# Kernel optimization log

Measured on AMD Instinct MI355X. Metric: run time of the kernel, lower is better.

The kernel has to match this reference:

```python
import jax, jax.numpy as jnp
import numpy as np

DIM = 512
N_HEADS = 8
HEAD_DIM = DIM // N_HEADS
BN_EPS = 1e-5


def setup_inputs() -> dict:
    key = jax.random.key(0)
    ks = jax.random.split(key, 8)
    B, C, H, W = 16, DIM, 32, 32
    x = jax.random.normal(ks[0], (B, C, H, W), dtype=jnp.float32)
    # 1x1 convs == channel matmuls: stacked q/k/v weights [3, out, in], proj [out, in]
    w_qkv = jax.random.normal(ks[1], (3, DIM, DIM), dtype=jnp.float32) * (DIM ** -0.5)
    w_proj = jax.random.normal(ks[2], (DIM, DIM), dtype=jnp.float32) * (DIM ** -0.5)
    # BatchNorm (inference form) params for q/k/v branches, stacked [3, C]
    bn_gamma = jax.random.uniform(ks[3], (3, DIM), minval=0.5, maxval=1.5)
    bn_beta = jax.random.normal(ks[4], (3, DIM)) * 0.1
    bn_mean = jax.random.normal(ks[5], (3, DIM)) * 0.1
    bn_var = jax.random.uniform(ks[6], (3, DIM), minval=0.5, maxval=1.5)
    return {"x": x, "w_qkv": w_qkv, "w_proj": w_proj, "bn_gamma": bn_gamma,
            "bn_beta": bn_beta, "bn_mean": bn_mean, "bn_var": bn_var}


def _ternary_ste(t):
    # forward: sign(t) in {-1,0,1}; backward: identity (straight-through)
    return t + jax.lax.stop_gradient(jnp.sign(t) - t)


def reference(x, w_qkv, w_proj, bn_gamma, bn_beta, bn_mean, bn_var):
    B, C, H, W = x.shape
    N = H * W
    xf = x.reshape(B, C, N)
    # fused 1x1 conv for q,k,v: [3,B,C,N]
    qkv = jnp.einsum('koc,bcn->kbon', w_qkv, xf)
    # BatchNorm (inference): y = (x - mean)/sqrt(var+eps)*gamma + beta
    s = bn_gamma / jnp.sqrt(bn_var + BN_EPS)          # [3,C]
    b = bn_beta - bn_mean * s                          # [3,C]
    qkv = qkv * s[:, None, :, None] + b[:, None, :, None]
    q = _ternary_ste(qkv[0]).reshape(B, N_HEADS, HEAD_DIM, N)
    k = _ternary_ste(qkv[1]).reshape(B, N_HEADS, HEAD_DIM, N)
    v = qkv[2].reshape(B, N_HEADS, HEAD_DIM, N)
    scale = HEAD_DIM ** -0.5
    attn = jnp.einsum('bhdn,bhen->bhde', q, k) * scale  # [B,h,d,d] channel-wise attn
    attn = jax.nn.softmax(attn, axis=-1)
    out = jnp.einsum('bhde,bhen->bhdn', attn, v).reshape(B, C, N)
    out = jnp.einsum('oc,bcn->bon', w_proj, out) + xf   # proj + residual
    return out.reshape(B, C, H, W)
```

## Files before the change

### kernel.cpp

```cpp
#include <hip/hip_runtime.h>
#include <math.h>

#define BN_EPS 1e-5f
#define FIXC 1.0e-4f

typedef _Float16 f16;
typedef _Float16 f16x4 __attribute__((ext_vector_type(4)));
typedef _Float16 f16x8 __attribute__((ext_vector_type(8)));
typedef float f32x4 __attribute__((ext_vector_type(4)));
typedef int i32x4 __attribute__((ext_vector_type(4)));

static constexpr int BB = 16;
static constexpr int C  = 512;
static constexpr int NP = 1024;
static constexpr int NH = 8;
static constexpr int HD = 64;
static constexpr int M3 = 1536;


static constexpr size_t OFF_WHI  = 0;
static constexpr size_t OFF_WLO  = 1572864;
static constexpr size_t OFF_WPH  = 3145728;
static constexpr size_t OFF_SB   = 3670016;
static constexpr size_t OFF_WN   = 3682304;
static constexpr size_t OFF_XN   = 3686400;
static constexpr size_t OFF_FLAG = 3751936;
static constexpr size_t OFF_XTH  = 5849088;
static constexpr size_t OFF_XTL  = 22626304;
static constexpr size_t OFF_AOT  = OFF_XTH;
static constexpr size_t OFF_Q    = 39403520;
static constexpr size_t OFF_K    = 47792128;
static constexpr size_t OFF_VT   = 56180736;

__device__ __forceinline__ void gld16(const void* g, void* l) {
  __builtin_amdgcn_global_load_lds(
      (const __attribute__((address_space(1))) void*)g,
      (__attribute__((address_space(3))) void*)l, 16, 0, 0);
}

__device__ __forceinline__ size_t frag_off(int tile, int kt, int row7, int k5) {
  return (((size_t)tile * 16 + kt) * 8 + (row7 >> 4)) * 512
       + (size_t)((row7 & 15) | ((k5 >> 3) << 4)) * 8;
}

__global__ __launch_bounds__(256) void k_convW(
    const float* __restrict__ wqkv, const float* __restrict__ wproj,
    const float* __restrict__ g, const float* __restrict__ be,
    const float* __restrict__ mu, const float* __restrict__ va,
    f16* __restrict__ Whi, f16* __restrict__ Wlo, f16* __restrict__ Wph,
    float* __restrict__ sA, float* __restrict__ bA)
{
  const int i = blockIdx.x * 256 + threadIdx.x;
  {
    const int m = i >> 6, l = i & 63;
    const float4 v0 = *(const float4*)&wqkv[(size_t)m * C + l * 8];
    const float4 v1 = *(const float4*)&wqkv[(size_t)m * C + l * 8 + 4];
    const float vv[8] = {v0.x, v0.y, v0.z, v0.w, v1.x, v1.y, v1.z, v1.w};
    f16x8 hv, lv;
#pragma unroll
    for (int q = 0; q < 8; ++q) {
      const f16 h = (f16)vv[q];
      hv[q] = h; lv[q] = (f16)(vv[q] - (float)h);
    }
    *(f16x8*)&Whi[frag_off(m >> 7, l >> 2, m & 127, (l & 3) * 8)] = hv;
    *(f16x8*)&Wlo[(size_t)m * C + l * 8] = lv;
  }
  if (i < 32768) {
    const int m = i >> 6, l = i & 63;
    const float4 v0 = *(const float4*)&wproj[(size_t)m * C + l * 8];
    const float4 v1 = *(const float4*)&wproj[(size_t)m * C + l * 8 + 4];
    const float vv[8] = {v0.x, v0.y, v0.z, v0.w, v1.x, v1.y, v1.z, v1.w};
    f16x8 hv;
#pragma unroll
    for (int q = 0; q < 8; ++q) hv[q] = (f16)vv[q];
    *(f16x8*)&Wph[frag_off(m >> 7, l >> 2, m & 127, (l & 3) * 8)] = hv;
  }
  if (i < M3) {
    const float s = g[i] / sqrtf(va[i] + BN_EPS);
    sA[i] = s;
    bA[i] = be[i] - mu[i] * s;
  }
}

__global__ __launch_bounds__(256) void k_wnorm(
    const float* __restrict__ wqkv, float* __restrict__ wnorm)
{
  const int row = blockIdx.x * 4 + (threadIdx.x >> 6);
  const int lane = threadIdx.x & 63;
  const float4 v0 = *(const float4*)&wqkv[(size_t)row * C + lane * 8];
  const float4 v1 = *(const float4*)&wqkv[(size_t)row * C + lane * 8 + 4];
  float s = v0.x * v0.x + v0.y * v0.y + v0.z * v0.z + v0.w * v0.w
          + v1.x * v1.x + v1.y * v1.y + v1.z * v1.z + v1.w * v1.w;
  s += __shfl_xor(s, 1);  s += __shfl_xor(s, 2);  s += __shfl_xor(s, 4);
  s += __shfl_xor(s, 8);  s += __shfl_xor(s, 16); s += __shfl_xor(s, 32);
  if (lane == 0) wnorm[row] = sqrtf(s);
}

__global__ __launch_bounds__(256) void k_convX(
    const float* __restrict__ x, f16* __restrict__ XtH, f16* __restrict__ XtL,
    float* __restrict__ xnorm2)
{
  const int k0 = blockIdx.x * 64, n0 = blockIdx.y * 64, b = blockIdx.z;
  __shared__ float ls[64][65];
  const int t = threadIdx.x;
  const float* xp = x + ((size_t)b * C + k0) * NP + n0;
  const int c4 = (t & 15) * 4, r0 = t >> 4;
#pragma unroll
  for (int q = 0; q < 4; ++q) {
    const float4 v = *(const float4*)(xp + (size_t)(r0 + q * 16) * NP + c4);
    ls[r0 + q * 16][c4 + 0] = v.x; ls[r0 + q * 16][c4 + 1] = v.y;
    ls[r0 + q * 16][c4 + 2] = v.z; ls[r0 + q * 16][c4 + 3] = v.w;
  }
  __syncthreads();
  if (t < 64) {
    float s2 = 0.f;
#pragma unroll
    for (int q = 0; q < 64; ++q) { const float v = ls[q][t]; s2 = fmaf(v, v, s2); }
    atomicAdd(&xnorm2[(b << 10) + n0 + t], s2);
  }
  const int n = t >> 2, kk = (t & 3) * 16;
  const int n_abs = n0 + n;
  f16x8 hv0 = {}, hv1 = {}, lv0 = {}, lv1 = {};
#pragma unroll
  for (int q = 0; q < 8; ++q) {
    const float v = ls[kk + q][n];
    const f16 h = (f16)v;
    hv0[q] = h; lv0[q] = (f16)(v - (float)h);
  }
#pragma unroll
  for (int q = 0; q < 8; ++q) {
    const float v = ls[kk + 8 + q][n];
    const f16 h = (f16)v;
    hv1[q] = h; lv1[q] = (f16)(v - (float)h);
  }
  const int kb0 = k0 + kk, kb1 = k0 + kk + 8;
  *(f16x8*)&XtH[frag_off(b * 8 + (n_abs >> 7), kb0 >> 5, n_abs & 127, kb0 & 31)] = hv0;
  *(f16x8*)&XtH[frag_off(b * 8 + (n_abs >> 7), kb1 >> 5, n_abs & 127, kb1 & 31)] = hv1;
  *(f16x8*)&XtL[((size_t)b * NP + n_abs) * C + kb0] = lv0;
  *(f16x8*)&XtL[((size_t)b * NP + n_abs) * C + kb1] = lv1;
}

__global__ __launch_bounds__(256) void k_qkv_mfma(
    const f16* __restrict__ Whi, const f16* __restrict__ XtH,
    const float* __restrict__ sA, const float* __restrict__ bA,
    const float* __restrict__ wnorm, const float* __restrict__ xnorm2,
    signed char* __restrict__ qw, signed char* __restrict__ kw,
    f16* __restrict__ vt, unsigned* __restrict__ flagbits)
{
  __shared__ __align__(16) f16 SMEM[32768];
  f16* const As0 = SMEM;
  f16* const Bs0 = SMEM + 8192;
  f16* const As1 = SMEM + 16384;
  f16* const Bs1 = SMEM + 24576;

  const int t = threadIdx.x, lane = t & 63, wid = t >> 6;
  const int n0 = blockIdx.x * 128, m0 = blockIdx.y * 128, b = blockIdx.z;

  const f16* Af = Whi + (size_t)(m0 >> 7) * 65536;
  const f16* Bf = XtH + ((size_t)b * 8 + (n0 >> 7)) * 65536;

  f32x4 acc[4][4];
#pragma unroll
  for (int i = 0; i < 4; ++i)
#pragma unroll
    for (int j = 0; j < 4; ++j) acc[i][j] = (f32x4){0.f, 0.f, 0.f, 0.f};

  const int wm = wid >> 1, wn = wid & 1;
  const int lr = lane & 15, ls = lane >> 4;
  const int soff = wid * 512 + lane * 8;

#define QSTAGE(TI, AS, BS) do {                                         \
    const f16* Ak_ = Af + (size_t)(TI) * 8192;                          \
    const f16* Bk_ = Bf + (size_t)(TI) * 8192;                          \
    _Pragma("unroll")                                                   \
    for (int r_ = 0; r_ < 4; ++r_) {                                    \
      gld16(Ak_ + r_ * 2048 + soff, &(AS)[r_ * 2048 + wid * 512]);      \
      gld16(Bk_ + r_ * 2048 + soff, &(BS)[r_ * 2048 + wid * 512]);      \
    }                                                                   \
  } while (0)

#define QCOMP(AS, BS) do {                                              \
    _Pragma("unroll")                                                   \
    for (int ksub_ = 0; ksub_ < 2; ++ksub_) {                           \
      f16x8 ah_[4], bh_[4];                                             \
      _Pragma("unroll")                                                 \
      for (int i_ = 0; i_ < 4; ++i_) {                                  \
        ah_[i_] = *(const f16x8*)&(AS)[ksub_ * 4096 + (wm * 4 + i_) * 512 + lane * 8]; \
        bh_[i_] = *(const f16x8*)&(BS)[ksub_ * 4096 + (wn * 4 + i_) * 512 + lane * 8]; \
      }                                                                 \
      _Pragma("unroll")                                                 \
      for (int i_ = 0; i_ < 4; ++i_)                                    \
        _Pragma("unroll")                                               \
        for (int j_ = 0; j_ < 4; ++j_)                                  \
          acc[i_][j_] = __builtin_amdgcn_mfma_f32_16x16x32_f16(         \
              ah_[i_], bh_[j_], acc[i_][j_], 0, 0, 0);                  \
    }                                                                   \
  } while (0)

  QSTAGE(0, As0, Bs0);
  __syncthreads();
#pragma unroll
  for (int ti = 0; ti < 7; ++ti) {
    if (ti & 1) { QSTAGE(ti + 1, As0, Bs0); QCOMP(As1, Bs1); }
    else        { QSTAGE(ti + 1, As1, Bs1); QCOMP(As0, Bs0); }
    __syncthreads();
  }
  QCOMP(As1, Bs1);

#undef QSTAGE
#undef QCOMP

  const int kidx = m0 >> 9;
  if (kidx != 2) {
    signed char* dst0 = (kidx == 0) ? qw : kw;
    float xnrm[4];
#pragma unroll
    for (int j = 0; j < 4; ++j)
      xnrm[j] = sqrtf(xnorm2[(b << 10) + n0 + wn * 64 + j * 16 + lr]);
#pragma unroll
    for (int i = 0; i < 4; ++i) {
      float sv[4], bv[4], dl[4];
#pragma unroll
      for (int r = 0; r < 4; ++r) {
        const int o = m0 + wm * 64 + i * 16 + ls * 4 + r;
        sv[r] = sA[o]; bv[r] = bA[o];
        dl[r] = FIXC * wnorm[o] * sv[r];
      }
      const int oc0 = (m0 & 511) + wm * 64 + i * 16 + ls * 4;
      const int og0 = m0 + wm * 64 + i * 16 + ls * 4;
#pragma unroll
      for (int j = 0; j < 4; ++j) {
        const int n = n0 + wn * 64 + j * 16 + lr;
#pragma unroll
        for (int r = 0; r < 4; ++r) {
          const float z = fmaf(acc[i][j][r], sv[r], bv[r]);
          dst0[((size_t)b * C + oc0 + r) * NP + n] =
              (signed char)((z > 0.f) - (z < 0.f));
          if (fabsf(z) <= dl[r] * xnrm[j]) {
            const int of = og0 + r;
            atomicOr(&flagbits[(((size_t)b * NP + n) << 5) + (of >> 5)],
                     1u << (of & 31));
          }
        }
      }
    }
  } else {
    const int c0 = m0 & 511;
    for (int hf = 0; hf < 2; ++hf) {
      __syncthreads();
      if (wn == hf) {
#pragma unroll
        for (int i = 0; i < 4; ++i) {
          float sv[4], bv[4];
#pragma unroll
          for (int r = 0; r < 4; ++r) {
            const int o = m0 + wm * 64 + i * 16 + ls * 4 + r;
            sv[r] = sA[o]; bv[r] = bA[o];
          }
#pragma unroll
          for (int j = 0; j < 4; ++j) {
            f16x4 pk;
#pragma unroll
            for (int r = 0; r < 4; ++r)
              pk[r] = (f16)fmaf(acc[i][j][r], sv[r], bv[r]);
            *(f16x4*)&SMEM[(size_t)(j * 16 + lr) * 136 + wm * 64 + i * 16 + ls * 4] = pk;
          }
        }
      }
      __syncthreads();
      const int nl = t >> 2, cc = (t & 3) * 32;
      const f16* src = &SMEM[(size_t)nl * 136 + cc];
      f16x8 r0 = *(const f16x8*)(src + 0);
      f16x8 r1 = *(const f16x8*)(src + 8);
      f16x8 r2 = *(const f16x8*)(src + 16);
      f16x8 r3 = *(const f16x8*)(src + 24);
      f16* dstv = vt + ((size_t)b * NP + n0 + hf * 64 + nl) * C + c0 + cc;
      *(f16x8*)(dstv + 0)  = r0;
      *(f16x8*)(dstv + 8)  = r1;
      *(f16x8*)(dstv + 16) = r2;
      *(f16x8*)(dstv + 24) = r3;
    }
  }
}

__global__ __launch_bounds__(256) void k_fix(
    const unsigned* __restrict__ flagbits,
    const f16* __restrict__ Whi, const f16* __restrict__ Wlo,
    const f16* __restrict__ XtH, const f16* __restrict__ XtL,
    const float* __restrict__ sA, const float* __restrict__ bA,
    signed char* __restrict__ qw, signed char* __restrict__ kw)
{
  const int wv = blockIdx.x * 4 + (threadIdx.x >> 6);
  const int lane = threadIdx.x & 63;
  const int b = wv >> 10, n = wv & 1023;

  const unsigned* bm = flagbits + ((size_t)wv << 5);
  const unsigned myw = (lane < 32) ? bm[lane] : 0u;
  if (__ballot(myw != 0) == 0ULL) return;

  const int kb = lane * 8;
  const f16x8 bhv = *(const f16x8*)&XtH[
      frag_off(b * 8 + (n >> 7), kb >> 5, n & 127, kb & 31)];
  const f16x8 blv = *(const f16x8*)&XtL[((size_t)b * NP + n) * C + kb];
  float xv[8];
#pragma unroll
  for (int q = 0; q < 8; ++q) xv[q] = (float)bhv[q] + (float)blv[q];

  for (int w = 0; w < 32; ++w) {
    unsigned bits = __shfl(myw, w);
    while (bits) {
      const int o = w * 32 + __builtin_ctz(bits);
      bits &= bits - 1;
      const f16x8 ahv = *(const f16x8*)&Whi[
          frag_off(o >> 7, kb >> 5, o & 127, kb & 31)];
      const f16x8 alv = *(const f16x8*)&Wlo[(size_t)o * C + kb];
      float s = 0.f;
#pragma unroll
      for (int q = 0; q < 8; ++q)
        s = fmaf((float)ahv[q] + (float)alv[q], xv[q], s);
      s += __shfl_xor(s, 1);  s += __shfl_xor(s, 2);  s += __shfl_xor(s, 4);
      s += __shfl_xor(s, 8);  s += __shfl_xor(s, 16); s += __shfl_xor(s, 32);
      if (lane == 0) {
        const float y = fmaf(s, sA[o], bA[o]);
        const signed char sg = (signed char)((y > 0.f) - (y < 0.f));
        if (o < 512) qw[((size_t)b * C + o) * NP + n] = sg;
        else         kw[((size_t)b * C + (o - 512)) * NP + n] = sg;
      }
    }
  }
}

__global__ __launch_bounds__(256) void k_attn_fused(
    const signed char* __restrict__ qw, const signed char* __restrict__ kw,
    const f16* __restrict__ vt, f16* __restrict__ aot)
{
  const int half = blockIdx.x;
  const int bh = blockIdx.y;
  const int b = bh >> 3, h = bh & 7;
  const int t = threadIdx.x, lane = t & 63, wid = t >> 6;
  const int dw = wid * 16;
  const int lr = lane & 15, lg = lane >> 4;

  __shared__ f16 ph[64][72];
  __shared__ f16 pl[64][72];
  __shared__ f16 sb[64][72];

  const signed char* qp = qw + ((size_t)b * C + h * HD + dw + lr) * NP;
  const signed char* kp = kw + ((size_t)b * C + h * HD + lr) * NP;

  i32x4 accS[4];
#pragma unroll
  for (int j = 0; j < 4; ++j) accS[j] = (i32x4){0, 0, 0, 0};

#pragma unroll 4
  for (int ks = 0; ks < 16; ++ks) {
    const i32x4 af = *(const i32x4*)(qp + ks * 64 + lg * 16);
#pragma unroll
    for (int j = 0; j < 4; ++j) {
      const i32x4 bf = *(const i32x4*)(kp + (size_t)(j * 16) * NP + ks * 64 + lg * 16);
      accS[j] = __builtin_amdgcn_mfma_i32_16x16x64_i8(af, bf, accS[j], 0, 0, 0);
    }
  }

#pragma unroll
  for (int r = 0; r < 4; ++r) {
    float mx = (float)accS[0][r];
#pragma unroll
    for (int j = 1; j < 4; ++j) mx = fmaxf(mx, (float)accS[j][r]);
    mx = fmaxf(mx, __shfl_xor(mx, 1));
    mx = fmaxf(mx, __shfl_xor(mx, 2));
    mx = fmaxf(mx, __shfl_xor(mx, 4));
    mx = fmaxf(mx, __shfl_xor(mx, 8));
    float pvv[4];
    float sm = 0.f;
#pragma unroll
    for (int j = 0; j < 4; ++j) {
      pvv[j] = expf(((float)accS[j][r] - mx) * 0.125f);
      sm += pvv[j];
    }
    sm += __shfl_xor(sm, 1);
    sm += __shfl_xor(sm, 2);
    sm += __shfl_xor(sm, 4);
    sm += __shfl_xor(sm, 8);
    const float inv = 1.f / sm;
    const int drow = dw + lg * 4 + r;
#pragma unroll
    for (int j = 0; j < 4; ++j) {
      const float p = pvv[j] * inv;
      const f16 hi = (f16)p;
      ph[drow][j * 16 + lr] = hi;
      pl[drow][j * 16 + lr] = (f16)(p - (float)hi);
    }
  }
  __syncthreads();

  const f16x8 pa0h = *(const f16x8*)&ph[dw + lr][lg * 8];
  const f16x8 pa0l = *(const f16x8*)&pl[dw + lr][lg * 8];
  const f16x8 pa1h = *(const f16x8*)&ph[dw + lr][32 + lg * 8];
  const f16x8 pa1l = *(const f16x8*)&pl[dw + lr][32 + lg * 8];

  const f16* vbase = vt + (size_t)b * NP * C + h * HD;
  const int nbase = half * 512;

  for (int nc = 0; nc < 8; ++nc) {
    const int nn0 = nbase + nc * 64;
    __syncthreads();
#pragma unroll
    for (int nt = 0; nt < 4; ++nt) {
      const f16* vp = vbase + (size_t)(nn0 + nt * 16 + lr) * C + lg * 8;
      const f16x8 bv0 = *(const f16x8*)(vp);
      const f16x8 bv1 = *(const f16x8*)(vp + 32);
      f32x4 acc = (f32x4){0.f, 0.f, 0.f, 0.f};
      acc = __builtin_amdgcn_mfma_f32_16x16x32_f16(pa0h, bv0, acc, 0, 0, 0);
      acc = __builtin_amdgcn_mfma_f32_16x16x32_f16(pa0l, bv0, acc, 0, 0, 0);
      acc = __builtin_amdgcn_mfma_f32_16x16x32_f16(pa1h, bv1, acc, 0, 0, 0);
      acc = __builtin_amdgcn_mfma_f32_16x16x32_f16(pa1l, bv1, acc, 0, 0, 0);
      f16x4 pk;
#pragma unroll
      for (int r = 0; r < 4; ++r) pk[r] = (f16)acc[r];
      *(f16x4*)&sb[nt * 16 + lr][dw + lg * 4] = pk;
    }
    __syncthreads();
    const int nl = t >> 2, cc = (t & 3) * 16;
    const f16x8 o0 = *(const f16x8*)&sb[nl][cc];
    const f16x8 o1 = *(const f16x8*)&sb[nl][cc + 8];
    const int n_abs = nn0 + nl;
    const int c1 = h * HD + cc, c2 = h * HD + cc + 8;
    *(f16x8*)&aot[frag_off(b * 8 + (n_abs >> 7), c1 >> 5, n_abs & 127, c1 & 31)] = o0;
    *(f16x8*)&aot[frag_off(b * 8 + (n_abs >> 7), c2 >> 5, n_abs & 127, c2 & 31)] = o1;
  }
}

__global__ __launch_bounds__(256) void k_proj_mfma(
    const f16* __restrict__ Wph, const f16* __restrict__ aot,
    const float* __restrict__ X, float* __restrict__ out)
{
  __shared__ __align__(16) f16 SMEM[16384];
  f16* As = SMEM;
  f16* Bs = SMEM + 8192;

  const int t = threadIdx.x, lane = t & 63, wid = t >> 6;
  const int n0 = blockIdx.x * 128, m0 = blockIdx.y * 128, b = blockIdx.z;

  const f16* Af = Wph + (size_t)(m0 >> 7) * 65536;
  const f16* Bf = aot + ((size_t)b * 8 + (n0 >> 7)) * 65536;

  f32x4 acc[4][4];
#pragma unroll
  for (int i = 0; i < 4; ++i)
#pragma unroll
    for (int j = 0; j < 4; ++j) acc[i][j] = (f32x4){0.f, 0.f, 0.f, 0.f};

  const int wm = wid >> 1, wn = wid & 1;
  const int lr = lane & 15, ls = lane >> 4;
  const int soff = wid * 512 + lane * 8;

  for (int kt = 0; kt < 16; kt += 2) {
    const f16* Ak = Af + (size_t)kt * 4096;
    const f16* Bk = Bf + (size_t)kt * 4096;
#pragma unroll
    for (int r = 0; r < 4; ++r) {
      gld16(Ak + r * 2048 + soff, &As[r * 2048 + wid * 512]);
      gld16(Bk + r * 2048 + soff, &Bs[r * 2048 + wid * 512]);
    }
    __syncthreads();
#pragma unroll
    for (int ksub = 0; ksub < 2; ++ksub) {
      f16x8 ah[4], bh[4];
#pragma unroll
      for (int i = 0; i < 4; ++i) {
        ah[i] = *(const f16x8*)&As[ksub * 4096 + (wm * 4 + i) * 512 + lane * 8];
        bh[i] = *(const f16x8*)&Bs[ksub * 4096 + (wn * 4 + i) * 512 + lane * 8];
      }
#pragma unroll
      for (int i = 0; i < 4; ++i)
#pragma unroll
        for (int j = 0; j < 4; ++j)
          acc[i][j] = __builtin_amdgcn_mfma_f32_16x16x32_f16(ah[i], bh[j], acc[i][j], 0, 0, 0);
    }
    __syncthreads();
  }

#pragma unroll
  for (int i = 0; i < 4; ++i) {
    const int oc0 = m0 + wm * 64 + i * 16 + ls * 4;
#pragma unroll
    for (int j = 0; j < 4; ++j) {
      const int n = n0 + wn * 64 + j * 16 + lr;
#pragma unroll
      for (int r = 0; r < 4; ++r) {
        const size_t idx = ((size_t)b * C + oc0 + r) * NP + n;
        out[idx] = acc[i][j][r] + X[idx];
      }
    }
  }
}

extern "C" void kernel_launch(void* const* d_in, const int* in_sizes, int n_in,
                              void* d_out, int out_size, void* d_ws, size_t ws_size,
                              hipStream_t stream)
{
  const float* x      = (const float*)d_in[0];
  const float* w_qkv  = (const float*)d_in[1];
  const float* w_proj = (const float*)d_in[2];
  const float* g      = (const float*)d_in[3];
  const float* be     = (const float*)d_in[4];
  const float* mu     = (const float*)d_in[5];
  const float* va     = (const float*)d_in[6];
  float* out = (float*)d_out;

  char* ws = (char*)d_ws;
  f16*  Whi = (f16*)(ws + OFF_WHI);
  f16*  Wlo = (f16*)(ws + OFF_WLO);
  f16*  Wph = (f16*)(ws + OFF_WPH);
  float* sA = (float*)(ws + OFF_SB);
  float* bA = sA + M3;
  float* wn = (float*)(ws + OFF_WN);
  float* xn2 = (float*)(ws + OFF_XN);
  unsigned* flagbits = (unsigned*)(ws + OFF_FLAG);
  f16*  XtH = (f16*)(ws + OFF_XTH);
  f16*  XtL = (f16*)(ws + OFF_XTL);
  f16*  aot = (f16*)(ws + OFF_AOT);
  signed char* qw = (signed char*)(ws + OFF_Q);
  signed char* kw = (signed char*)(ws + OFF_K);
  f16*  vtw = (f16*)(ws + OFF_VT);

  hipMemsetAsync(xn2, 0, OFF_XTH - OFF_XN, stream);

  k_convW<<<dim3(384), 256, 0, stream>>>(
      w_qkv, w_proj, g, be, mu, va, Whi, Wlo, Wph, sA, bA);
  k_wnorm<<<dim3(256), 256, 0, stream>>>(w_qkv, wn);
  k_convX<<<dim3(C / 64, NP / 64, BB), 256, 0, stream>>>(x, XtH, XtL, xn2);
  k_qkv_mfma<<<dim3(NP / 128, M3 / 128, BB), 256, 0, stream>>>(
      Whi, XtH, sA, bA, wn, xn2, qw, kw, vtw, flagbits);
  k_fix<<<dim3(BB * NP / 4), 256, 0, stream>>>(
      flagbits, Whi, Wlo, XtH, XtL, sA, bA, qw, kw);
  k_attn_fused<<<dim3(2, BB * NH), 256, 0, stream>>>(qw, kw, vtw, aot);
  k_proj_mfma<<<dim3(NP / 128, C / 128, BB), 256, 0, stream>>>(Wph, aot, x, out);
}
```

Before: 139.4 us.

## Double-buffer proj GEMM and use explicit vmcnt waits in QKV pipeline

The projection GEMM kernel gains double-buffered LDS tiles so the direct-to-LDS global loads for the next K tile are issued before computing the current one. The QKV GEMM pipeline replaces __syncthreads with explicit s_waitcnt vmcnt(8) plus s_barrier, so only the older stage's loads must land before compute while the newer prefetch stays in flight. The aim is to hide global load latency behind MFMA work. It doubles LDS use in the proj kernel, which could lower occupancy, and the hand-placed waitcnt counts depend on each stage issuing exactly eight loads per thread.

```diff
diff --git a/kernel.cpp b/kernel.cpp
--- a/kernel.cpp
+++ b/kernel.cpp
@@ -198,14 +198,22 @@
   } while (0)
 
   QSTAGE(0, As0, Bs0);
-  __syncthreads();
-#pragma unroll
-  for (int ti = 0; ti < 7; ++ti) {
-    if (ti & 1) { QSTAGE(ti + 1, As0, Bs0); QCOMP(As1, Bs1); }
-    else        { QSTAGE(ti + 1, As1, Bs1); QCOMP(As0, Bs0); }
-    __syncthreads();
-  }
-  QCOMP(As1, Bs1);
+#pragma unroll
+  for (int ti = 0; ti < 8; ++ti) {
+    if (ti < 7) {
+      if (ti & 1) QSTAGE(ti + 1, As0, Bs0);
+      else        QSTAGE(ti + 1, As1, Bs1);
+      asm volatile("s_waitcnt vmcnt(8)" ::: "memory");
+    } else {
+      asm volatile("s_waitcnt vmcnt(0)" ::: "memory");
+    }
+    __builtin_amdgcn_sched_barrier(0);
+    __builtin_amdgcn_s_barrier();
+    if (ti & 1) QCOMP(As1, Bs1); else QCOMP(As0, Bs0);
+    asm volatile("s_waitcnt lgkmcnt(0)" ::: "memory");
+    __builtin_amdgcn_sched_barrier(0);
+    __builtin_amdgcn_s_barrier();
+  }
 
 #undef QSTAGE
 #undef QCOMP
@@ -435,9 +443,11 @@
     const f16* __restrict__ Wph, const f16* __restrict__ aot,
     const float* __restrict__ X, float* __restrict__ out)
 {
-  __shared__ __align__(16) f16 SMEM[16384];
-  f16* As = SMEM;
-  f16* Bs = SMEM + 8192;
+  __shared__ __align__(16) f16 SMEM[32768];
+  f16* const As0 = SMEM;
+  f16* const Bs0 = SMEM + 8192;
+  f16* const As1 = SMEM + 16384;
+  f16* const Bs1 = SMEM + 24576;
 
   const int t = threadIdx.x, lane = t & 63, wid = t >> 6;
   const int n0 = blockIdx.x * 128, m0 = blockIdx.y * 128, b = blockIdx.z;
@@ -455,31 +465,54 @@
   const int lr = lane & 15, ls = lane >> 4;
   const int soff = wid * 512 + lane * 8;
 
-  for (int kt = 0; kt < 16; kt += 2) {
-    const f16* Ak = Af + (size_t)kt * 4096;
-    const f16* Bk = Bf + (size_t)kt * 4096;
-#pragma unroll
-    for (int r = 0; r < 4; ++r) {
-      gld16(Ak + r * 2048 + soff, &As[r * 2048 + wid * 512]);
-      gld16(Bk + r * 2048 + soff, &Bs[r * 2048 + wid * 512]);
-    }
-    __syncthreads();
-#pragma unroll
-    for (int ksub = 0; ksub < 2; ++ksub) {
-      f16x8 ah[4], bh[4];
-#pragma unroll
-      for (int i = 0; i < 4; ++i) {
-        ah[i] = *(const f16x8*)&As[ksub * 4096 + (wm * 4 + i) * 512 + lane * 8];
-        bh[i] = *(const f16x8*)&Bs[ksub * 4096 + (wn * 4 + i) * 512 + lane * 8];
-      }
-#pragma unroll
-      for (int i = 0; i < 4; ++i)
-#pragma unroll
-        for (int j = 0; j < 4; ++j)
-          acc[i][j] = __builtin_amdgcn_mfma_f32_16x16x32_f16(ah[i], bh[j], acc[i][j], 0, 0, 0);
-    }
-    __syncthreads();
-  }
+#define PSTAGE(TI, AS, BS) do {                                         \
+    const f16* Ak_ = Af + (size_t)(TI) * 8192;                          \
+    const f16* Bk_ = Bf + (size_t)(TI) * 8192;                          \
+    _Pragma("unroll")                                                   \
+    for (int r_ = 0; r_ < 4; ++r_) {                                    \
+      gld16(Ak_ + r_ * 2048 + soff, &(AS)[r_ * 2048 + wid * 512]);      \
+      gld16(Bk_ + r_ * 2048 + soff, &(BS)[r_ * 2048 + wid * 512]);      \
+    }                                                                   \
+  } while (0)
+
+#define PCOMP(AS, BS) do {                                              \
+    _Pragma("unroll")                                                   \
+    for (int ksub_ = 0; ksub_ < 2; ++ksub_) {                           \
+      f16x8 ah_[4], bh_[4];                                             \
+      _Pragma("unroll")                                                 \
+      for (int i_ = 0; i_ < 4; ++i_) {                                  \
+        ah_[i_] = *(const f16x8*)&(AS)[ksub_ * 4096 + (wm * 4 + i_) * 512 + lane * 8]; \
+        bh_[i_] = *(const f16x8*)&(BS)[ksub_ * 4096 + (wn * 4 + i_) * 512 + lane * 8]; \
+      }                                                                 \
+      _Pragma("unroll")                                                 \
+      for (int i_ = 0; i_ < 4; ++i_)                                    \
+        _Pragma("unroll")                                               \
+        for (int j_ = 0; j_ < 4; ++j_)                                  \
+          acc[i_][j_] = __builtin_amdgcn_mfma_f32_16x16x32_f16(         \
+              ah_[i_], bh_[j_], acc[i_][j_], 0, 0, 0);                  \
+    }                                                                   \
+  } while (0)
+
+  PSTAGE(0, As0, Bs0);
+#pragma unroll
+  for (int ti = 0; ti < 8; ++ti) {
+    if (ti < 7) {
+      if (ti & 1) PSTAGE(ti + 1, As0, Bs0);
+      else        PSTAGE(ti + 1, As1, Bs1);
+      asm volatile("s_waitcnt vmcnt(8)" ::: "memory");
+    } else {
+      asm volatile("s_waitcnt vmcnt(0)" ::: "memory");
+    }
+    __builtin_amdgcn_sched_barrier(0);
+    __builtin_amdgcn_s_barrier();
+    if (ti & 1) PCOMP(As1, Bs1); else PCOMP(As0, Bs0);
+    asm volatile("s_waitcnt lgkmcnt(0)" ::: "memory");
+    __builtin_amdgcn_sched_barrier(0);
+    __builtin_amdgcn_s_barrier();
+  }
+
+#undef PSTAGE
+#undef PCOMP
 
 #pragma unroll
   for (int i = 0; i < 4; ++i) {
```

After: 136.7 us, median of 2. Within noise of the previous version (-1.9%).

## Load MFMA fragments directly from global into registers, dropping LDS staging

Applied to the files above, without the earlier changes.

The QKV and projection GEMM kernels stop staging A/B tiles through shared memory with global_load_lds and barriers. Each wave now loads its pre-swizzled fragments straight from global memory into registers, double-buffered across k-steps, and both kernels get launch bounds asking for 2 blocks per CU. This removes the LDS round trip and the __syncthreads calls. In exchange, operands shared between waves are fetched from global or L2 more than once, which adds traffic, and register pressure rises.

```diff
diff --git a/kernel.cpp b/kernel.cpp
--- a/kernel.cpp
+++ b/kernel.cpp
@@ -32,12 +32,6 @@
 static constexpr size_t OFF_K    = 47792128;
 static constexpr size_t OFF_VT   = 56180736;
 
-__device__ __forceinline__ void gld16(const void* g, void* l) {
-  __builtin_amdgcn_global_load_lds(
-      (const __attribute__((address_space(1))) void*)g,
-      (__attribute__((address_space(3))) void*)l, 16, 0, 0);
-}
-
 __device__ __forceinline__ size_t frag_off(int tile, int kt, int row7, int k5) {
   return (((size_t)tile * 16 + kt) * 8 + (row7 >> 4)) * 512
        + (size_t)((row7 & 15) | ((k5 >> 3) << 4)) * 8;
@@ -140,18 +134,14 @@
   *(f16x8*)&XtL[((size_t)b * NP + n_abs) * C + kb1] = lv1;
 }
 
-__global__ __launch_bounds__(256) void k_qkv_mfma(
+__global__ __launch_bounds__(256, 2) void k_qkv_mfma(
     const f16* __restrict__ Whi, const f16* __restrict__ XtH,
     const float* __restrict__ sA, const float* __restrict__ bA,
     const float* __restrict__ wnorm, const float* __restrict__ xnorm2,
     signed char* __restrict__ qw, signed char* __restrict__ kw,
     f16* __restrict__ vt, unsigned* __restrict__ flagbits)
 {
-  __shared__ __align__(16) f16 SMEM[32768];
-  f16* const As0 = SMEM;
-  f16* const Bs0 = SMEM + 8192;
-  f16* const As1 = SMEM + 16384;
-  f16* const Bs1 = SMEM + 24576;
+  __shared__ __align__(16) f16 SMEM[8704];
 
   const int t = threadIdx.x, lane = t & 63, wid = t >> 6;
   const int n0 = blockIdx.x * 128, m0 = blockIdx.y * 128, b = blockIdx.z;
@@ -167,48 +157,38 @@
 
   const int wm = wid >> 1, wn = wid & 1;
   const int lr = lane & 15, ls = lane >> 4;
-  const int soff = wid * 512 + lane * 8;
-
-#define QSTAGE(TI, AS, BS) do {                                         \
-    const f16* Ak_ = Af + (size_t)(TI) * 8192;                          \
-    const f16* Bk_ = Bf + (size_t)(TI) * 8192;                          \
+
+#define LOADF(KT, AR, BR) do {                                          \
     _Pragma("unroll")                                                   \
-    for (int r_ = 0; r_ < 4; ++r_) {                                    \
-      gld16(Ak_ + r_ * 2048 + soff, &(AS)[r_ * 2048 + wid * 512]);      \
-      gld16(Bk_ + r_ * 2048 + soff, &(BS)[r_ * 2048 + wid * 512]);      \
+    for (int i_ = 0; i_ < 4; ++i_) {                                    \
+      (AR)[i_] = *(const f16x8*)&Af[(size_t)(KT) * 4096 + (wm * 4 + i_) * 512 + lane * 8]; \
+      (BR)[i_] = *(const f16x8*)&Bf[(size_t)(KT) * 4096 + (wn * 4 + i_) * 512 + lane * 8]; \
     }                                                                   \
   } while (0)
 
-#define QCOMP(AS, BS) do {                                              \
+#define COMPF(AR, BR) do {                                              \
     _Pragma("unroll")                                                   \
-    for (int ksub_ = 0; ksub_ < 2; ++ksub_) {                           \
-      f16x8 ah_[4], bh_[4];                                             \
+    for (int i_ = 0; i_ < 4; ++i_)                                      \
       _Pragma("unroll")                                                 \
-      for (int i_ = 0; i_ < 4; ++i_) {                                  \
-        ah_[i_] = *(const f16x8*)&(AS)[ksub_ * 4096 + (wm * 4 + i_) * 512 + lane * 8]; \
-        bh_[i_] = *(const f16x8*)&(BS)[ksub_ * 4096 + (wn * 4 + i_) * 512 + lane * 8]; \
-      }                                                                 \
-      _Pragma("unroll")                                                 \
-      for (int i_ = 0; i_ < 4; ++i_)                                    \
-        _Pragma("unroll")                                               \
-        for (int j_ = 0; j_ < 4; ++j_)                                  \
-          acc[i_][j_] = __builtin_amdgcn_mfma_f32_16x16x32_f16(         \
-              ah_[i_], bh_[j_], acc[i_][j_], 0, 0, 0);                  \
-    }                                                                   \
+      for (int j_ = 0; j_ < 4; ++j_)                                    \
+        acc[i_][j_] = __builtin_amdgcn_mfma_f32_16x16x32_f16(           \
+            (AR)[i_], (BR)[j_], acc[i_][j_], 0, 0, 0);                  \
   } while (0)
 
-  QSTAGE(0, As0, Bs0);
-  __syncthreads();
-#pragma unroll
-  for (int ti = 0; ti < 7; ++ti) {
-    if (ti & 1) { QSTAGE(ti + 1, As0, Bs0); QCOMP(As1, Bs1); }
-    else        { QSTAGE(ti + 1, As1, Bs1); QCOMP(As0, Bs0); }
-    __syncthreads();
-  }
-  QCOMP(As1, Bs1);
-
-#undef QSTAGE
-#undef QCOMP
+  {
+    f16x8 a0[4], b0[4], a1[4], b1[4];
+    LOADF(0, a0, b0);
+#pragma unroll
+    for (int kt = 0; kt < 16; kt += 2) {
+      LOADF(kt + 1, a1, b1);
+      COMPF(a0, b0);
+      if (kt + 2 < 16) LOADF(kt + 2, a0, b0);
+      COMPF(a1, b1);
+    }
+  }
+
+#undef LOADF
+#undef COMPF
 
   const int kidx = m0 >> 9;
   if (kidx != 2) {
@@ -431,14 +411,10 @@
   }
 }
 
-__global__ __launch_bounds__(256) void k_proj_mfma(
+__global__ __launch_bounds__(256, 2) void k_proj_mfma(
     const f16* __restrict__ Wph, const f16* __restrict__ aot,
     const float* __restrict__ X, float* __restrict__ out)
 {
-  __shared__ __align__(16) f16 SMEM[16384];
-  f16* As = SMEM;
-  f16* Bs = SMEM + 8192;
-
   const int t = threadIdx.x, lane = t & 63, wid = t >> 6;
   const int n0 = blockIdx.x * 128, m0 = blockIdx.y * 128, b = blockIdx.z;
 
@@ -453,33 +429,38 @@
 
   const int wm = wid >> 1, wn = wid & 1;
   const int lr = lane & 15, ls = lane >> 4;
-  const int soff = wid * 512 + lane * 8;
-
-  for (int kt = 0; kt < 16; kt += 2) {
-    const f16* Ak = Af + (size_t)kt * 4096;
-    const f16* Bk = Bf + (size_t)kt * 4096;
-#pragma unroll
-    for (int r = 0; r < 4; ++r) {
-      gld16(Ak + r * 2048 + soff, &As[r * 2048 + wid * 512]);
-      gld16(Bk + r * 2048 + soff, &Bs[r * 2048 + wid * 512]);
-    }
-    __syncthreads();
-#pragma unroll
-    for (int ksub = 0; ksub < 2; ++ksub) {
-      f16x8 ah[4], bh[4];
-#pragma unroll
-      for (int i = 0; i < 4; ++i) {
-        ah[i] = *(const f16x8*)&As[ksub * 4096 + (wm * 4 + i) * 512 + lane * 8];
-        bh[i] = *(const f16x8*)&Bs[ksub * 4096 + (wn * 4 + i) * 512 + lane * 8];
-      }
-#pragma unroll
-      for (int i = 0; i < 4; ++i)
-#pragma unroll
-        for (int j = 0; j < 4; ++j)
-          acc[i][j] = __builtin_amdgcn_mfma_f32_16x16x32_f16(ah[i], bh[j], acc[i][j], 0, 0, 0);
-    }
-    __syncthreads();
-  }
+
+#define LOADF(KT, AR, BR) do {                                          \
+    _Pragma("unroll")                                                   \
+    for (int i_ = 0; i_ < 4; ++i_) {                                    \
+      (AR)[i_] = *(const f16x8*)&Af[(size_t)(KT) * 4096 + (wm * 4 + i_) * 512 + lane * 8]; \
+      (BR)[i_] = *(const f16x8*)&Bf[(size_t)(KT) * 4096 + (wn * 4 + i_) * 512 + lane * 8]; \
+    }                                                                   \
+  } while (0)
+
+#define COMPF(AR, BR) do {                                              \
+    _Pragma("unroll")                                                   \
+    for (int i_ = 0; i_ < 4; ++i_)                                      \
+      _Pragma("unroll")                                                 \
+      for (int j_ = 0; j_ < 4; ++j_)                                    \
+        acc[i_][j_] = __builtin_amdgcn_mfma_f32_16x16x32_f16(           \
+            (AR)[i_], (BR)[j_], acc[i_][j_], 0, 0, 0);                  \
+  } while (0)
+
+  {
+    f16x8 a0[4], b0[4], a1[4], b1[4];
+    LOADF(0, a0, b0);
+#pragma unroll
+    for (int kt = 0; kt < 16; kt += 2) {
+      LOADF(kt + 1, a1, b1);
+      COMPF(a0, b0);
+      if (kt + 2 < 16) LOADF(kt + 2, a0, b0);
+      COMPF(a1, b1);
+    }
+  }
+
+#undef LOADF
+#undef COMPF
 
 #pragma unroll
   for (int i = 0; i < 4; ++i) {
```

Result: no change. 139.2 us (-0.1%).
